# Performance work log

Hardware: AMD Instinct MI355X
Metric: run time of the kernel (lower is better)

The kernel has to match this reference:

```python
import jax, jax.numpy as jnp
import numpy as np

B, N, K, C = 4, 4096, 16, 128
BN_EPS = 1e-5


def setup_inputs() -> dict:
    key = jax.random.key(0)
    ks = jax.random.split(key, 16)
    def f(i, shape, s=0.05):
        return jax.random.normal(ks[i], shape, dtype=jnp.float32) * s
    return dict(
        pose_enc=f(0, (B, N, K, 4), 1.0),
        knn_idx=jax.random.randint(ks[1], (B, N, K), 0, N),
        new_points=f(2, (B, N, C), 1.0),
        wq=f(3, (C, C)), wk=f(4, (C, C)), wv=f(5, (C, C)),
        g_w1=f(6, (C, C)), g_b1=jnp.zeros((C,), jnp.float32),
        g_w2=f(7, (C, C)), g_b2=jnp.zeros((C,), jnp.float32),
        d_w1=f(8, (C, 4)), d_b1=jnp.zeros((C,), jnp.float32),
        d_w2=f(9, (C, C)), d_b2=jnp.zeros((C,), jnp.float32),
        c1_w=f(10, (C, C)), c1_b=jnp.zeros((C,), jnp.float32),
        bn1_g=jnp.ones((C,), jnp.float32), bn1_b=jnp.zeros((C,), jnp.float32),
        c2_w=f(11, (C, C)), c2_b=jnp.zeros((C,), jnp.float32),
        bn2_g=jnp.ones((C,), jnp.float32), bn2_b=jnp.zeros((C,), jnp.float32),
    )


def _bn(x, g, b):
    # BatchNorm1d in training mode: stats over (B, N) per channel, biased var
    m = jnp.mean(x, axis=(0, 1))
    v = jnp.mean(jnp.square(x - m), axis=(0, 1))
    return (x - m) * jax.lax.rsqrt(v + BN_EPS) * g + b


def reference(pose_enc, knn_idx, new_points, wq, wk, wv,
              g_w1, g_b1, g_w2, g_b2, d_w1, d_b1, d_w2, d_b2,
              c1_w, c1_b, bn1_g, bn1_b, c2_w, c2_b, bn2_g, bn2_b):
    # fc_delta: (B,N,K,4) -> (B,N,K,C)
    pos = jax.nn.relu(pose_enc @ d_w1.T + d_b1) @ d_w2.T + d_b2
    # CONV2 (1x1 conv == per-point linear) + BN + ReLU on new_points
    x = jax.nn.relu(_bn(new_points @ c2_w.T + c2_b, bn2_g, bn2_b))  # (B,N,C)
    q = x @ wq.T                                   # (B,N,C)
    kf = x @ wk.T
    vf = x @ wv.T
    gather = jax.vmap(lambda pts, idx: pts[idx])   # (B,N,C),(B,N,K)->(B,N,K,C)
    kk = gather(kf, knn_idx)
    vv = gather(vf, knn_idx)
    # fc_gamma vector attention scores
    h = q[:, :, None, :] - kk + pos                # (B,N,K,C)
    attn = jax.nn.relu(h @ g_w1.T + g_b1) @ g_w2.T + g_b2
    # NOTE: original divides by sqrt(k.size(-1)) where k is the key tensor -> sqrt(C)
    attn = jax.nn.softmax(attn / jnp.sqrt(jnp.float32(C)), axis=-2)
    res = jnp.einsum('bmnf,bmnf->bmf', attn, vv + pos)  # (B,N,C)
    res = jax.nn.relu(_bn(res @ c1_w.T + c1_b, bn1_g, bn1_b)) + new_points
    return res
```

## Files before the change

### kernel.cpp

```cpp
#include <hip/hip_runtime.h>
#include <hip/hip_bf16.h>

typedef __bf16 bf16;
typedef __bf16 bf16x4 __attribute__((ext_vector_type(4)));
typedef __bf16 bf16x8 __attribute__((ext_vector_type(8)));
typedef float  f32x4  __attribute__((ext_vector_type(4)));

#define NN 4096
#define KK 16
#define CC 128
#define BN_TOT 16384

__global__ __launch_bounds__(256) void k_lin(
    const float* __restrict__ A, const float* __restrict__ W,
    const float* __restrict__ bias, float* __restrict__ Y,
    float* __restrict__ partial) {
  __shared__ __attribute__((aligned(16))) bf16 WF[16 * 64 * 8];
  __shared__ __attribute__((aligned(16))) float SF[4][16][68];
  __shared__ float P1[64], P2[64];
  int tid = threadIdx.x, w = tid >> 6, l = tid & 63, quad = l >> 4, col = l & 15;
  int rb = blockIdx.x >> 1, ch = blockIdx.x & 1;
  int r0 = rb * 64, cbase = ch * 64;
  int arow = r0 + w * 16 + col;

  if (tid < 64) { P1[tid] = 0.f; P2[tid] = 0.f; }

  for (int e = tid; e < 64 * 16; e += 256) {
    int r = e >> 4, c8 = e & 15;
    const float* p = W + (cbase + r) * CC + c8 * 8;
    f32x4 v0 = *(const f32x4*)p, v1 = *(const f32x4*)(p + 4);
    bf16x8 o;
    for (int i = 0; i < 4; i++) { o[i] = (bf16)v0[i]; o[i + 4] = (bf16)v1[i]; }
    int chunk = (r >> 4) * 4 + (c8 >> 2);
    int lane  = (c8 & 3) * 16 + (r & 15);
    *(bf16x8*)(&WF[(chunk * 64 + lane) * 8]) = o;
  }

  bf16x8 a[4];
  for (int kc = 0; kc < 4; kc++) {
    int c0 = kc * 32 + quad * 8;
    f32x4 y0 = *(const f32x4*)(A + arow * CC + c0);
    f32x4 y1 = *(const f32x4*)(A + arow * CC + c0 + 4);
    bf16x8 o;
    for (int i = 0; i < 4; i++) { o[i] = (bf16)y0[i]; o[i + 4] = (bf16)y1[i]; }
    a[kc] = o;
  }

  f32x4 D[4];
  for (int jb = 0; jb < 4; jb++) {
    float bv = bias[cbase + jb * 16 + col];
    D[jb] = (f32x4){bv, bv, bv, bv};
  }
  __syncthreads();
  for (int jb = 0; jb < 4; jb++)
    for (int kc = 0; kc < 4; kc++) {
      bf16x8 bfrag = *(const bf16x8*)(&WF[((jb * 4 + kc) * 64 + l) * 8]);
      D[jb] = __builtin_amdgcn_mfma_f32_16x16x32_bf16(a[kc], bfrag, D[jb], 0, 0, 0);
    }

  for (int jb = 0; jb < 4; jb++) {
    float t1 = D[jb][0] + D[jb][1] + D[jb][2] + D[jb][3];
    float t2 = D[jb][0] * D[jb][0] + D[jb][1] * D[jb][1]
             + D[jb][2] * D[jb][2] + D[jb][3] * D[jb][3];
    t1 += __shfl_xor(t1, 16); t1 += __shfl_xor(t1, 32);
    t2 += __shfl_xor(t2, 16); t2 += __shfl_xor(t2, 32);
    if (quad == 0) {
      atomicAdd(&P1[jb * 16 + col], t1);
      atomicAdd(&P2[jb * 16 + col], t2);
    }
  }

  for (int jb = 0; jb < 4; jb++)
    for (int g = 0; g < 4; g++)
      SF[w][quad * 4 + g][jb * 16 + col] = D[jb][g];
  int orow = r0 + w * 16 + (l >> 2), oc = (l & 3) * 16;
  for (int c4 = 0; c4 < 4; c4++) {
    f32x4 v = *(const f32x4*)(&SF[w][l >> 2][oc + c4 * 4]);
    *(f32x4*)(Y + orow * CC + cbase + oc + c4 * 4) = v;
  }

  __syncthreads();
  if (tid < 64) {
    partial[blockIdx.x * 128 + tid] = P1[tid];
    partial[blockIdx.x * 128 + 64 + tid] = P2[tid];
  }
}

__global__ __launch_bounds__(256) void k_finalize(
    const float* __restrict__ partial, const float* __restrict__ g,
    const float* __restrict__ b, float* __restrict__ stats) {
  __shared__ float sh[2][16][16];
  int t = threadIdx.x, cl = t & 15, gr = t >> 4;
  int c = blockIdx.x * 16 + cl;
  int ch = c >> 6, j = c & 63;
  float s1 = 0.f, s2 = 0.f;
  for (int rb = gr; rb < 256; rb += 16) {
    const float* pp = partial + (rb * 2 + ch) * 128;
    s1 += pp[j];
    s2 += pp[64 + j];
  }
  sh[0][gr][cl] = s1; sh[1][gr][cl] = s2;
  __syncthreads();
  if (t < 16) {
    s1 = 0.f; s2 = 0.f;
    for (int hh = 0; hh < 16; hh++) {
      s1 += sh[0][hh][t];
      s2 += sh[1][hh][t];
    }
    int cc = blockIdx.x * 16 + t;
    float mean = s1 * (1.0f / BN_TOT);
    float var  = s2 * (1.0f / BN_TOT) - mean * mean;
    float r = rsqrtf(var + 1e-5f);
    float sc = g[cc] * r;
    stats[cc] = sc;
    stats[128 + cc] = b[cc] - mean * sc;
  }
}

__global__ __launch_bounds__(256) void k_qkv(
    const float* __restrict__ Y, const float* __restrict__ stats,
    const float* __restrict__ Wq, const float* __restrict__ Wk, const float* __restrict__ Wv,
    bf16* __restrict__ Qo, bf16* __restrict__ Ko, bf16* __restrict__ Vo) {
  __shared__ __attribute__((aligned(16))) bf16 WF[32 * 64 * 8];
  __shared__ __attribute__((aligned(16))) bf16 S[4][16][132];
  int tid = threadIdx.x, w = tid >> 6, l = tid & 63, quad = l >> 4, col = l & 15;
  int j8 = blockIdx.x >> 3, x8 = blockIdx.x & 7;
  int m = j8 >> 5;
  int rb = x8 * 32 + (j8 & 31);
  int r0 = rb * 64;
  int arow = r0 + w * 16 + col;
  const float* Wg = (m == 0) ? Wq : (m == 1) ? Wk : Wv;
  bf16* Os = (m == 0) ? Qo : (m == 1) ? Ko : Vo;

  for (int e = tid; e < 128 * 16; e += 256) {
    int r = e >> 4, c8 = e & 15;
    const float* p = Wg + r * CC + c8 * 8;
    f32x4 v0 = *(const f32x4*)p, v1 = *(const f32x4*)(p + 4);
    bf16x8 o;
    for (int i = 0; i < 4; i++) { o[i] = (bf16)v0[i]; o[i + 4] = (bf16)v1[i]; }
    int chunk = (r >> 4) * 4 + (c8 >> 2);
    int lane  = (c8 & 3) * 16 + (r & 15);
    *(bf16x8*)(&WF[(chunk * 64 + lane) * 8]) = o;
  }

  bf16x8 a[4];
  for (int kc = 0; kc < 4; kc++) {
    int c0 = kc * 32 + quad * 8;
    f32x4 y0  = *(const f32x4*)(Y + arow * CC + c0);
    f32x4 y1  = *(const f32x4*)(Y + arow * CC + c0 + 4);
    f32x4 sc0 = *(const f32x4*)(stats + c0);
    f32x4 sc1 = *(const f32x4*)(stats + c0 + 4);
    f32x4 sf0 = *(const f32x4*)(stats + 128 + c0);
    f32x4 sf1 = *(const f32x4*)(stats + 128 + c0 + 4);
    bf16x8 o;
    for (int i = 0; i < 4; i++) {
      o[i]     = (bf16)fmaxf(y0[i] * sc0[i] + sf0[i], 0.f);
      o[i + 4] = (bf16)fmaxf(y1[i] * sc1[i] + sf1[i], 0.f);
    }
    a[kc] = o;
  }

  __syncthreads();
  f32x4 D[8];
  for (int jb = 0; jb < 8; jb++) D[jb] = (f32x4){0.f, 0.f, 0.f, 0.f};
  for (int jb = 0; jb < 8; jb++)
    for (int kc = 0; kc < 4; kc++) {
      bf16x8 bfrag = *(const bf16x8*)(&WF[((jb * 4 + kc) * 64 + l) * 8]);
      D[jb] = __builtin_amdgcn_mfma_f32_16x16x32_bf16(a[kc], bfrag, D[jb], 0, 0, 0);
    }
  for (int jb = 0; jb < 8; jb++)
    for (int g = 0; g < 4; g++)
      S[w][quad * 4 + g][jb * 16 + col] = (bf16)D[jb][g];
  int orow = r0 + w * 16 + (l >> 2), oc0 = (l & 3) * 32;
  for (int c8 = 0; c8 < 4; c8++) {
    bf16x8 v = *(const bf16x8*)(&S[w][l >> 2][oc0 + c8 * 8]);
    *(bf16x8*)(Os + orow * CC + oc0 + c8 * 8) = v;
  }
}

__global__ __launch_bounds__(512) void k_attn(
    const bf16* __restrict__ Q, const bf16* __restrict__ Kf, const bf16* __restrict__ Vf,
    const int* __restrict__ knn, const float* __restrict__ pose,
    const float* __restrict__ d_w1, const float* __restrict__ d_b1,
    const float* __restrict__ d_w2, const float* __restrict__ d_b2,
    const float* __restrict__ g_w1, const float* __restrict__ g_b1,
    const float* __restrict__ g_w2, const float* __restrict__ g_b2,
    float* __restrict__ Rs) {
  __shared__ __attribute__((aligned(16))) bf16 WF[104 * 64 * 8];
  __shared__ __attribute__((aligned(16))) bf16 S[8][16][132];
  __shared__ float BSf[512];

  int tid = threadIdx.x, w = tid >> 6, l = tid & 63, quad = l >> 4, col = l & 15;
  int bid = (blockIdx.x & 7) * 32 + (blockIdx.x >> 3);

  const float* Wg3[3] = {d_w2, g_w1, g_w2};
  for (int m = 0; m < 3; m++) {
    const float* Wg = Wg3[m];
    for (int e = tid; e < 128 * 16; e += 512) {
      int r = e >> 4, c8 = e & 15;
      const float* p = Wg + r * CC + c8 * 8;
      f32x4 v0 = *(const f32x4*)p, v1 = *(const f32x4*)(p + 4);
      bf16x8 o;
      for (int i = 0; i < 4; i++) { o[i] = (bf16)v0[i]; o[i + 4] = (bf16)v1[i]; }
      int chunk = m * 32 + (r >> 4) * 4 + (c8 >> 2);
      int lane  = (c8 & 3) * 16 + (r & 15);
      *(bf16x8*)(&WF[(chunk * 64 + lane) * 8]) = o;
    }
  }
  for (int e = tid; e < 8 * 64; e += 512) {
    int jb = e >> 6, lane = e & 63, q = lane >> 4, c = lane & 15;
    bf16x8 o;
    for (int i = 0; i < 8; i++) o[i] = (bf16)0.f;
    if (q == 0) {
      f32x4 v = *(const f32x4*)(d_w1 + (jb * 16 + c) * 4);
      for (int i = 0; i < 4; i++) o[i] = (bf16)v[i];
    }
    *(bf16x8*)(&WF[((96 + jb) * 64 + lane) * 8]) = o;
  }
  if (tid < 512) {
    const float* bp = (tid < 128) ? d_b1 : (tid < 256) ? d_b2
                     : (tid < 384) ? g_b1 : g_b2;
    BSf[tid] = bp[tid & 127];
  }
  __syncthreads();

  const float smc = 0.08838834764831845f;

  int gpf = bid * 64 + w * 8;
  int i16 = knn[gpf * KK + col];
  f32x4 ps = *(const f32x4*)(pose + gpf * 64 + col * 4);

#pragma unroll 1
  for (int p = 0; p < 8; p++) {
    int gp = bid * 64 + w * 8 + p;
    int b  = gp >> 12;

    int vidx[4];
#pragma unroll
    for (int g = 0; g < 4; g++) vidx[g] = __shfl(i16, quad * 4 + g);
    float vv[8][4];
#pragma unroll
    for (int g = 0; g < 4; g++) {
      const bf16* vr = Vf + ((b << 12) + vidx[g]) * CC + col;
#pragma unroll
      for (int jb = 0; jb < 8; jb++) vv[jb][g] = (float)vr[jb * 16];
    }
    int grow = (b << 12) + i16;

    bf16x8 ap;
#pragma unroll
    for (int j = 0; j < 8; j++) ap[j] = (bf16)0.f;
    if (quad == 0) {
#pragma unroll
      for (int j = 0; j < 4; j++) ap[j] = (bf16)ps[j];
    }
    f32x4 D[8];
#pragma unroll
    for (int jb = 0; jb < 8; jb++) {
      float bv = BSf[jb * 16 + col];
      D[jb] = (f32x4){bv, bv, bv, bv};
      bf16x8 bfrag = *(const bf16x8*)(&WF[((96 + jb) * 64 + l) * 8]);
      D[jb] = __builtin_amdgcn_mfma_f32_16x16x32_bf16(ap, bfrag, D[jb], 0, 0, 0);
    }
#pragma unroll
    for (int jb = 0; jb < 8; jb++)
#pragma unroll
      for (int g = 0; g < 4; g++)
        S[w][quad * 4 + g][jb * 16 + col] = (bf16)fmaxf(D[jb][g], 0.f);
    bf16x8 aA[4];
#pragma unroll
    for (int kc = 0; kc < 4; kc++)
      aA[kc] = *(const bf16x8*)(&S[w][col][kc * 32 + quad * 8]);

    bf16x8 kkv[4];
#pragma unroll
    for (int kc = 0; kc < 4; kc++)
      kkv[kc] = *(const bf16x8*)(Kf + grow * CC + kc * 32 + quad * 8);

    if (p < 7) {
      i16 = knn[(gp + 1) * KK + col];
      ps  = *(const f32x4*)(pose + (gp + 1) * 64 + col * 4);
    }

#pragma unroll
    for (int jb = 0; jb < 8; jb++) {
      float bv = BSf[128 + jb * 16 + col];
      D[jb] = (f32x4){bv, bv, bv, bv};
    }
#pragma unroll
    for (int jb = 0; jb < 8; jb++)
#pragma unroll
      for (int kc = 0; kc < 4; kc++) {
        bf16x8 bfrag = *(const bf16x8*)(&WF[((jb * 4 + kc) * 64 + l) * 8]);
        D[jb] = __builtin_amdgcn_mfma_f32_16x16x32_bf16(aA[kc], bfrag, D[jb], 0, 0, 0);
      }

#pragma unroll
    for (int jb = 0; jb < 8; jb++)
#pragma unroll
      for (int g = 0; g < 4; g++) vv[jb][g] += D[jb][g];

#pragma unroll
    for (int jb = 0; jb < 8; jb++)
#pragma unroll
      for (int g = 0; g < 4; g++)
        S[w][quad * 4 + g][jb * 16 + col] = (bf16)D[jb][g];
#pragma unroll
    for (int kc = 0; kc < 4; kc++) {
      int c0 = kc * 32 + quad * 8;
      bf16x8 qv = *(const bf16x8*)(Q + gp * CC + c0);
      bf16x8 pv = *(const bf16x8*)(&S[w][col][c0]);
      bf16x8 hv;
#pragma unroll
      for (int j = 0; j < 8; j++)
        hv[j] = (bf16)((float)qv[j] - (float)kkv[kc][j] + (float)pv[j]);
      aA[kc] = hv;
    }

#pragma unroll
    for (int jb = 0; jb < 8; jb++) {
      float bv = BSf[256 + jb * 16 + col];
      D[jb] = (f32x4){bv, bv, bv, bv};
    }
#pragma unroll
    for (int jb = 0; jb < 8; jb++)
#pragma unroll
      for (int kc = 0; kc < 4; kc++) {
        bf16x8 bfrag = *(const bf16x8*)(&WF[((32 + jb * 4 + kc) * 64 + l) * 8]);
        D[jb] = __builtin_amdgcn_mfma_f32_16x16x32_bf16(aA[kc], bfrag, D[jb], 0, 0, 0);
      }
#pragma unroll
    for (int jb = 0; jb < 8; jb++)
#pragma unroll
      for (int g = 0; g < 4; g++)
        S[w][quad * 4 + g][jb * 16 + col] = (bf16)fmaxf(D[jb][g], 0.f);
#pragma unroll
    for (int kc = 0; kc < 4; kc++)
      aA[kc] = *(const bf16x8*)(&S[w][col][kc * 32 + quad * 8]);

#pragma unroll
    for (int jb = 0; jb < 8; jb++) {
      float bv = BSf[384 + jb * 16 + col];
      D[jb] = (f32x4){bv, bv, bv, bv};
    }
#pragma unroll
    for (int jb = 0; jb < 8; jb++)
#pragma unroll
      for (int kc = 0; kc < 4; kc++) {
        bf16x8 bfrag = *(const bf16x8*)(&WF[((64 + jb * 4 + kc) * 64 + l) * 8]);
        D[jb] = __builtin_amdgcn_mfma_f32_16x16x32_bf16(aA[kc], bfrag, D[jb], 0, 0, 0);
      }

#pragma unroll
    for (int jb = 0; jb < 8; jb++) {
      float s = 0.f, pa = 0.f;
#pragma unroll
      for (int g = 0; g < 4; g++) {
        float e = __expf(D[jb][g] * smc);
        s += e; pa += e * vv[jb][g];
      }
      s  += __shfl_xor(s, 16);  s += __shfl_xor(s, 32);
      pa += __shfl_xor(pa, 16); pa += __shfl_xor(pa, 32);
      if (quad == 0) Rs[gp * CC + jb * 16 + col] = pa / s;
    }
  }
}

__global__ __launch_bounds__(256) void k_out(
    const float* __restrict__ Y, const float* __restrict__ stats,
    const float* __restrict__ NP, float* __restrict__ Out) {
  int i0 = (blockIdx.x * 256 + threadIdx.x) * 4;
  int c0 = i0 & 127;
  f32x4 y  = *(const f32x4*)(Y + i0);
  f32x4 sc = *(const f32x4*)(stats + c0);
  f32x4 sh = *(const f32x4*)(stats + 128 + c0);
  f32x4 np = *(const f32x4*)(NP + i0);
  f32x4 o;
  for (int i = 0; i < 4; i++)
    o[i] = fmaxf(y[i] * sc[i] + sh[i], 0.f) + np[i];
  *(f32x4*)(Out + i0) = o;
}

__global__ void k_code(float* out, float code) {
  if (threadIdx.x == 0) out[1000003] = code;
}

extern "C" void kernel_launch(void* const* d_in, const int* in_sizes, int n_in,
                              void* d_out, int out_size, void* d_ws, size_t ws_size,
                              hipStream_t stream) {
  static const int expect[22] = {
    1048576, 262144, 2097152, 16384, 16384, 16384,
    16384, 128, 16384, 128,
    512, 128, 16384, 128,
    16384, 128, 128, 128,
    16384, 128, 128, 128
  };
  if (n_in != 22) { k_code<<<1, 64, 0, stream>>>((float*)d_out, 4194304.f); return; }
  for (int i = 0; i < 22; i++)
    if (in_sizes[i] != expect[i]) {
      k_code<<<1, 64, 0, stream>>>((float*)d_out, 262144.f * (float)(i + 1));
      return;
    }

  const float* pose  = (const float*)d_in[0];
  const int*   knn   = (const int*)d_in[1];
  const float* np_   = (const float*)d_in[2];
  const float* wq    = (const float*)d_in[3];
  const float* wk    = (const float*)d_in[4];
  const float* wv    = (const float*)d_in[5];
  const float* g_w1  = (const float*)d_in[6];
  const float* g_b1  = (const float*)d_in[7];
  const float* g_w2  = (const float*)d_in[8];
  const float* g_b2  = (const float*)d_in[9];
  const float* d_w1  = (const float*)d_in[10];
  const float* d_b1  = (const float*)d_in[11];
  const float* d_w2  = (const float*)d_in[12];
  const float* d_b2  = (const float*)d_in[13];
  const float* c1_w  = (const float*)d_in[14];
  const float* c1_b  = (const float*)d_in[15];
  const float* bn1_g = (const float*)d_in[16];
  const float* bn1_b = (const float*)d_in[17];
  const float* c2_w  = (const float*)d_in[18];
  const float* c2_b  = (const float*)d_in[19];
  const float* bn2_g = (const float*)d_in[20];
  const float* bn2_b = (const float*)d_in[21];

  float* y2      = (float*)d_ws;
  float* res     = y2 + 2097152;
  bf16*  qf      = (bf16*)(res + 2097152);
  bf16*  kf      = qf + 2097152;
  bf16*  vf      = kf + 2097152;
  float* partial = (float*)(vf + 2097152);
  float* stats2  = partial + 65536;
  float* stats1  = stats2 + 256;

  size_t NEED = (size_t)((char*)(stats1 + 256) - (char*)d_ws);
  if (ws_size < NEED) {
    k_code<<<1, 64, 0, stream>>>((float*)d_out, 2097152.f);
    return;
  }

  k_lin     <<<512, 256, 0, stream>>>(np_, c2_w, c2_b, y2, partial);
  k_finalize<<<8, 256, 0, stream>>>(partial, bn2_g, bn2_b, stats2);
  k_qkv     <<<768, 256, 0, stream>>>(y2, stats2, wq, wk, wv, qf, kf, vf);
  k_attn    <<<256, 512, 0, stream>>>(qf, kf, vf, knn, pose,
                                      d_w1, d_b1, d_w2, d_b2,
                                      g_w1, g_b1, g_w2, g_b2, res);
  k_lin     <<<512, 256, 0, stream>>>(res, c1_w, c1_b, y2, partial);
  k_finalize<<<8, 256, 0, stream>>>(partial, bn1_g, bn1_b, stats1);
  k_out     <<<2048, 256, 0, stream>>>(y2, stats1, np_, (float*)d_out);
}
```

Measured before the change: 204.2 us.

## Split QKV projection into half-width column blocks with register-resident weights

The QKV kernel now processes 64 output columns per block instead of 128, doubling the grid. Weights are loaded directly from global memory into MFMA B-fragments held in registers, which removes the shared-memory weight staging and its barrier. This adds register pressure and repeats each weight fragment load across all waves of a block and across more blocks, in exchange for less LDS use and more parallelism.

```diff
diff --git a/kernel.cpp b/kernel.cpp
--- a/kernel.cpp
+++ b/kernel.cpp
@@ -117,33 +117,36 @@
   }
 }
 
-__global__ __launch_bounds__(256) void k_qkv(
+__global__ __launch_bounds__(256, 1) void k_qkv(
     const float* __restrict__ Y, const float* __restrict__ stats,
     const float* __restrict__ Wq, const float* __restrict__ Wk, const float* __restrict__ Wv,
     bf16* __restrict__ Qo, bf16* __restrict__ Ko, bf16* __restrict__ Vo) {
-  __shared__ __attribute__((aligned(16))) bf16 WF[32 * 64 * 8];
-  __shared__ __attribute__((aligned(16))) bf16 S[4][16][132];
+  __shared__ __attribute__((aligned(16))) bf16 S[4][16][68];
   int tid = threadIdx.x, w = tid >> 6, l = tid & 63, quad = l >> 4, col = l & 15;
-  int j8 = blockIdx.x >> 3, x8 = blockIdx.x & 7;
-  int m = j8 >> 5;
-  int rb = x8 * 32 + (j8 & 31);
-  int r0 = rb * 64;
+  int x8 = blockIdx.x & 7, lj = blockIdx.x >> 3;
+  int rb = x8 * 32 + (lj & 31);
+  int mch = lj >> 5;
+  int m = mch >> 1, ch = mch & 1;
+  int r0 = rb * 64, cbase = ch * 64;
   int arow = r0 + w * 16 + col;
   const float* Wg = (m == 0) ? Wq : (m == 1) ? Wk : Wv;
   bf16* Os = (m == 0) ? Qo : (m == 1) ? Ko : Vo;
 
-  for (int e = tid; e < 128 * 16; e += 256) {
-    int r = e >> 4, c8 = e & 15;
-    const float* p = Wg + r * CC + c8 * 8;
-    f32x4 v0 = *(const f32x4*)p, v1 = *(const f32x4*)(p + 4);
-    bf16x8 o;
-    for (int i = 0; i < 4; i++) { o[i] = (bf16)v0[i]; o[i + 4] = (bf16)v1[i]; }
-    int chunk = (r >> 4) * 4 + (c8 >> 2);
-    int lane  = (c8 & 3) * 16 + (r & 15);
-    *(bf16x8*)(&WF[(chunk * 64 + lane) * 8]) = o;
-  }
+  bf16x8 bW[16];
+#pragma unroll
+  for (int jb = 0; jb < 4; jb++)
+#pragma unroll
+    for (int kc = 0; kc < 4; kc++) {
+      const float* p = Wg + (cbase + jb * 16 + col) * CC + kc * 32 + quad * 8;
+      f32x4 v0 = *(const f32x4*)p, v1 = *(const f32x4*)(p + 4);
+      bf16x8 o;
+#pragma unroll
+      for (int i = 0; i < 4; i++) { o[i] = (bf16)v0[i]; o[i + 4] = (bf16)v1[i]; }
+      bW[jb * 4 + kc] = o;
+    }
 
   bf16x8 a[4];
+#pragma unroll
   for (int kc = 0; kc < 4; kc++) {
     int c0 = kc * 32 + quad * 8;
     f32x4 y0  = *(const f32x4*)(Y + arow * CC + c0);
@@ -153,6 +156,7 @@
     f32x4 sf0 = *(const f32x4*)(stats + 128 + c0);
     f32x4 sf1 = *(const f32x4*)(stats + 128 + c0 + 4);
     bf16x8 o;
+#pragma unroll
     for (int i = 0; i < 4; i++) {
       o[i]     = (bf16)fmaxf(y0[i] * sc0[i] + sf0[i], 0.f);
       o[i + 4] = (bf16)fmaxf(y1[i] * sc1[i] + sf1[i], 0.f);
@@ -160,21 +164,25 @@
     a[kc] = o;
   }
 
-  __syncthreads();
-  f32x4 D[8];
-  for (int jb = 0; jb < 8; jb++) D[jb] = (f32x4){0.f, 0.f, 0.f, 0.f};
-  for (int jb = 0; jb < 8; jb++)
-    for (int kc = 0; kc < 4; kc++) {
-      bf16x8 bfrag = *(const bf16x8*)(&WF[((jb * 4 + kc) * 64 + l) * 8]);
-      D[jb] = __builtin_amdgcn_mfma_f32_16x16x32_bf16(a[kc], bfrag, D[jb], 0, 0, 0);
-    }
-  for (int jb = 0; jb < 8; jb++)
+  f32x4 D[4];
+#pragma unroll
+  for (int jb = 0; jb < 4; jb++) D[jb] = (f32x4){0.f, 0.f, 0.f, 0.f};
+#pragma unroll
+  for (int jb = 0; jb < 4; jb++)
+#pragma unroll
+    for (int kc = 0; kc < 4; kc++)
+      D[jb] = __builtin_amdgcn_mfma_f32_16x16x32_bf16(a[kc], bW[jb * 4 + kc], D[jb], 0, 0, 0);
+
+#pragma unroll
+  for (int jb = 0; jb < 4; jb++)
+#pragma unroll
     for (int g = 0; g < 4; g++)
       S[w][quad * 4 + g][jb * 16 + col] = (bf16)D[jb][g];
-  int orow = r0 + w * 16 + (l >> 2), oc0 = (l & 3) * 32;
-  for (int c8 = 0; c8 < 4; c8++) {
-    bf16x8 v = *(const bf16x8*)(&S[w][l >> 2][oc0 + c8 * 8]);
-    *(bf16x8*)(Os + orow * CC + oc0 + c8 * 8) = v;
+  int orow = r0 + w * 16 + (l >> 2), oc = (l & 3) * 16;
+#pragma unroll
+  for (int c8 = 0; c8 < 2; c8++) {
+    bf16x8 v = *(const bf16x8*)(&S[w][l >> 2][oc + c8 * 8]);
+    *(bf16x8*)(Os + orow * CC + cbase + oc + c8 * 8) = v;
   }
 }
 
@@ -442,7 +450,7 @@
 
   k_lin     <<<512, 256, 0, stream>>>(np_, c2_w, c2_b, y2, partial);
   k_finalize<<<8, 256, 0, stream>>>(partial, bn2_g, bn2_b, stats2);
-  k_qkv     <<<768, 256, 0, stream>>>(y2, stats2, wq, wk, wv, qf, kf, vf);
+  k_qkv     <<<1536, 256, 0, stream>>>(y2, stats2, wq, wk, wv, qf, kf, vf);
   k_attn    <<<256, 512, 0, stream>>>(qf, kf, vf, knn, pose,
                                       d_w1, d_b1, d_w2, d_b2,
                                       g_w1, g_b1, g_w2, g_b2, res);
```

Result: slower. 225.1 us (+10.2%).
